# Kernel tuning notes

Hardware: AMD Instinct MI355X
Metric: run time of the kernel (lower is better)

The kernel has to match this reference:

```python
import jax, jax.numpy as jnp
import numpy as np

B, C = 65536, 1000
EPS = float(np.finfo(np.float32).eps)

def setup_inputs() -> dict:
    key = jax.random.key(0)
    k1, k2, k3 = jax.random.split(key, 3)
    return {
        "Simple_vector": jax.random.normal(k1, (B, C), dtype=jnp.float32),
        "label_list": jax.random.randint(k2, (B,), 0, C),
        "w_L": jax.random.normal(k3, (C,), dtype=jnp.float32),
        "w_H": jnp.ones((1,), dtype=jnp.float32),
        "b": jnp.ones((1,), dtype=jnp.float32),
    }

def reference(Simple_vector, label_list, w_L, w_H, b):
    C_ = Simple_vector.shape[1]
    # LTS: per-row dot with class-weight vector
    LTS = Simple_vector @ w_L  # (B,)
    # H_hat = sum_i p_i * log p_i  (negative entropy), single stable pass
    logp = jax.nn.log_softmax(Simple_vector, axis=1)
    H_hat = jnp.sum(jnp.exp(logp) * logp, axis=1)  # (B,)
    HTS = w_H[0] * (H_hat / jnp.log(jnp.float32(C_))) + b[0]
    a = LTS + HTS
    T = jnp.clip(jax.nn.softplus(a), EPS, None)  # (B,)
    scaled = Simple_vector / T[:, None]
    # mean cross-entropy
    ls = jax.nn.log_softmax(scaled, axis=1)
    nll = -jnp.take_along_axis(ls, label_list[:, None], axis=1)[:, 0]
    return jnp.mean(nll)
```

## Files before the change

kernel.cpp:

```cpp
#include <hip/hip_runtime.h>
#include <float.h>
#include <math.h>


static constexpr int   kC4    = 250;
static constexpr int   kBlock = 256;
static constexpr int   kGrid  = 2048;
static constexpr int   kWavesTotal = kGrid * (kBlock / 64);
static constexpr int   kRPW   = 8;
static constexpr float kEps   = 1.1920928955078125e-07f;
static constexpr float kLogC  = 6.907755279f;

__device__ __forceinline__ float wred_max(float v) {
#pragma unroll
  for (int off = 32; off > 0; off >>= 1) v = fmaxf(v, __shfl_xor(v, off, 64));
  return v;
}
__device__ __forceinline__ float wred_sum(float v) {
#pragma unroll
  for (int off = 32; off > 0; off >>= 1) v += __shfl_xor(v, off, 64);
  return v;
}

__device__ __forceinline__ void p1_dot_max(const float4 c, const float4 w,
                                           float& L, float& m) {
  L = fmaf(c.x, w.x, L); L = fmaf(c.y, w.y, L);
  L = fmaf(c.z, w.z, L); L = fmaf(c.w, w.w, L);
  m = fmaxf(m, fmaxf(fmaxf(c.x, c.y), fmaxf(c.z, c.w)));
}
__device__ __forceinline__ void p2_raw(const float4 c, float& S, float& W) {
  float e;
  e = __expf(c.x); S += e; W = fmaf(e, c.x, W);
  e = __expf(c.y); S += e; W = fmaf(e, c.y, W);
  e = __expf(c.z); S += e; W = fmaf(e, c.z, W);
  e = __expf(c.w); S += e; W = fmaf(e, c.w, W);
}
__device__ __forceinline__ void p3_sumexp2(const float4 c, const float rT,
                                           const float nmrT, float& S2) {
  S2 += __expf(fmaf(c.x, rT, nmrT)); S2 += __expf(fmaf(c.y, rT, nmrT));
  S2 += __expf(fmaf(c.z, rT, nmrT)); S2 += __expf(fmaf(c.w, rT, nmrT));
}
__device__ __forceinline__ float pick_lab(const float4 v, const int el) {
  return (el == 0) ? v.x : (el == 1) ? v.y : (el == 2) ? v.z : v.w;
}

#define SENT4 make_float4(-FLT_MAX, -FLT_MAX, -FLT_MAX, -FLT_MAX)

__global__ __launch_bounds__(kBlock, 4) void ats_row_kernel_ns(
    const float* __restrict__ X, const int* __restrict__ labels,
    const float* __restrict__ wL, const float* __restrict__ wH,
    const float* __restrict__ bb, double* __restrict__ partial) {
  const int lane   = threadIdx.x & 63;
  const int wib    = threadIdx.x >> 6;
  const int wid    = blockIdx.x * (kBlock / 64) + wib;
  const bool tailok = lane < (kC4 - 192);

  const float4* WLr = reinterpret_cast<const float4*>(wL);
  const float4 w0 = WLr[lane];
  const float4 w1 = WLr[64 + lane];
  const float4 w2 = WLr[128 + lane];
  const float4 w3 = tailok ? WLr[192 + lane] : make_float4(0.f, 0.f, 0.f, 0.f);
  const float wH0 = wH[0];
  const float b0  = bb[0];

  double acc = 0.0;
  const int base = wid * kRPW;

  float4 a0, a1, a2, a3, b0_, b1_, b2_, b3_;
  int labA, labB;
  {
    const float4* Xa = reinterpret_cast<const float4*>(X) + (size_t)base * kC4;
    a0 = Xa[lane]; a1 = Xa[64 + lane]; a2 = Xa[128 + lane];
    a3 = tailok ? Xa[192 + lane] : SENT4;
    labA = labels[base];
    const float4* Xb = Xa + kC4;
    b0_ = Xb[lane]; b1_ = Xb[64 + lane]; b2_ = Xb[128 + lane];
    b3_ = tailok ? Xb[192 + lane] : SENT4;
    labB = labels[base + 1];
  }

  float4 pa0, pa1, pa2, pa3;
  float prT = 0.f, pnmrT = 0.f, pxl = 0.f;

#pragma unroll
  for (int i = 0; i < kRPW; ++i) {
    float4 n0 = SENT4, n1 = SENT4, n2 = SENT4, n3 = SENT4;
    int labN = 0;
    if (i + 2 < kRPW) {
      const float4* Xn =
          reinterpret_cast<const float4*>(X) + (size_t)(base + i + 2) * kC4;
      n0 = Xn[lane]; n1 = Xn[64 + lane]; n2 = Xn[128 + lane];
      n3 = tailok ? Xn[192 + lane] : SENT4;
      labN = labels[base + i + 2];
    }

    float L = 0.f, m = -FLT_MAX;
    p1_dot_max(a0, w0, L, m); p1_dot_max(a1, w1, L, m);
    p1_dot_max(a2, w2, L, m); p1_dot_max(a3, w3, L, m);

    float S = 0.f, W = 0.f;
    p2_raw(a0, S, W); p2_raw(a1, S, W);
    p2_raw(a2, S, W); p2_raw(a3, S, W);

    float S2p = 0.f;
    if (i > 0) {
      p3_sumexp2(pa0, prT, pnmrT, S2p); p3_sumexp2(pa1, prT, pnmrT, S2p);
      p3_sumexp2(pa2, prT, pnmrT, S2p); p3_sumexp2(pa3, prT, pnmrT, S2p);
    }

    const int c4l = labA >> 2;
    const int sl  = c4l >> 6, ln = c4l & 63, el = labA & 3;
    float4 v = (sl == 0) ? a0 : (sl == 1) ? a1 : (sl == 2) ? a2 : a3;
    const float xl = __shfl(pick_lab(v, el), ln, 64);

#pragma unroll
    for (int off = 32; off > 0; off >>= 1) {
      const float mo  = __shfl_xor(m,   off, 64);
      const float So  = __shfl_xor(S,   off, 64);
      const float Wo  = __shfl_xor(W,   off, 64);
      const float Lo  = __shfl_xor(L,   off, 64);
      const float S2o = __shfl_xor(S2p, off, 64);
      m = fmaxf(m, mo);
      S += So; W += Wo; L += Lo; S2p += S2o;
    }

    if (i > 0) acc += (double)(__logf(S2p) - fmaf(pxl, prT, pnmrT));

    const float Hhat = W / S - __logf(S);
    const float aT   = L + wH0 * (Hhat / kLogC) + b0;
    const float sp   = (aT > 0.f) ? (aT + log1pf(__expf(-aT)))
                                  : log1pf(__expf(aT));
    const float T    = fmaxf(sp, kEps);
    const float rT   = 1.0f / T;

    prT = rT; pnmrT = -m * rT; pxl = xl;
    pa0 = a0; pa1 = a1; pa2 = a2; pa3 = a3;

    a0 = b0_; a1 = b1_; a2 = b2_; a3 = b3_; labA = labB;
    b0_ = n0; b1_ = n1; b2_ = n2; b3_ = n3; labB = labN;
  }

  {
    float S2p = 0.f;
    p3_sumexp2(pa0, prT, pnmrT, S2p); p3_sumexp2(pa1, prT, pnmrT, S2p);
    p3_sumexp2(pa2, prT, pnmrT, S2p); p3_sumexp2(pa3, prT, pnmrT, S2p);
    S2p = wred_sum(S2p);
    acc += (double)(__logf(S2p) - fmaf(pxl, prT, pnmrT));
  }

  __shared__ double sacc[kBlock / 64];
  if (lane == 0) sacc[wib] = acc;
  __syncthreads();
  if (threadIdx.x == 0)
    partial[blockIdx.x] = (sacc[0] + sacc[1]) + (sacc[2] + sacc[3]);
}

__device__ __forceinline__ void p2_sumexp(const float4 c, const float m,
                                          float& S, float& W) {
  float e;
  e = __expf(c.x - m); S += e; W = fmaf(e, c.x, W);
  e = __expf(c.y - m); S += e; W = fmaf(e, c.y, W);
  e = __expf(c.z - m); S += e; W = fmaf(e, c.z, W);
  e = __expf(c.w - m); S += e; W = fmaf(e, c.w, W);
}
__device__ __forceinline__ float row_nll(
    const float4 c0, const float4 c1, const float4 c2, const float4 c3,
    const float4 w0, const float4 w1, const float4 w2, const float4 w3,
    const int labc, const float wH0, const float b0) {
  float L = 0.f, m = -FLT_MAX;
  p1_dot_max(c0, w0, L, m); p1_dot_max(c1, w1, L, m);
  p1_dot_max(c2, w2, L, m); p1_dot_max(c3, w3, L, m);
  m = wred_max(m);
  float S = 0.f, W = 0.f;
  p2_sumexp(c0, m, S, W); p2_sumexp(c1, m, S, W);
  p2_sumexp(c2, m, S, W); p2_sumexp(c3, m, S, W);
  S = wred_sum(S); W = wred_sum(W); L = wred_sum(L);
  const int c4l = labc >> 2;
  const int sl = c4l >> 6, ln = c4l & 63, el = labc & 3;
  float4 v = (sl == 0) ? c0 : (sl == 1) ? c1 : (sl == 2) ? c2 : c3;
  const float xl = __shfl(pick_lab(v, el), ln, 64);
  const float Hhat = W / S - m - __logf(S);
  const float a = L + wH0 * (Hhat / kLogC) + b0;
  const float sp = (a > 0.f) ? (a + log1pf(__expf(-a))) : log1pf(__expf(a));
  const float T = fmaxf(sp, kEps);
  const float rT = 1.0f / T, nmrT = -m * rT;
  float S2 = 0.f;
  p3_sumexp2(c0, rT, nmrT, S2); p3_sumexp2(c1, rT, nmrT, S2);
  p3_sumexp2(c2, rT, nmrT, S2); p3_sumexp2(c3, rT, nmrT, S2);
  S2 = wred_sum(S2);
  return __logf(S2) - fmaf(xl, rT, nmrT);
}

__global__ __launch_bounds__(kBlock) void ats_row_kernel_gen(
    const float* __restrict__ X, const int* __restrict__ labels,
    const float* __restrict__ wL, const float* __restrict__ wH,
    const float* __restrict__ bb, double* __restrict__ partial, int B) {
  const int lane   = threadIdx.x & 63;
  const int wib    = threadIdx.x >> 6;
  const int wid    = blockIdx.x * (kBlock / 64) + wib;
  const bool tailok = lane < (kC4 - 192);

  const float4* WLr = reinterpret_cast<const float4*>(wL);
  const float4 w0 = WLr[lane];
  const float4 w1 = WLr[64 + lane];
  const float4 w2 = WLr[128 + lane];
  const float4 w3 = tailok ? WLr[192 + lane] : make_float4(0.f, 0.f, 0.f, 0.f);
  const float wH0 = wH[0];
  const float b0  = bb[0];

  double acc = 0.0;
  int row = wid;
  float4 c0, c1, c2, c3;
  int labc = 0;
  if (row < B) {
    const float4* Xr = reinterpret_cast<const float4*>(X) + (size_t)row * kC4;
    c0 = Xr[lane]; c1 = Xr[64 + lane]; c2 = Xr[128 + lane];
    c3 = tailok ? Xr[192 + lane] : SENT4;
    labc = labels[row];
  }
  for (; row < B; row += kWavesTotal) {
    const int nrow = row + kWavesTotal;
    float4 n0 = SENT4, n1 = SENT4, n2 = SENT4, n3 = SENT4;
    int labn = 0;
    if (nrow < B) {
      const float4* Xn = reinterpret_cast<const float4*>(X) + (size_t)nrow * kC4;
      n0 = Xn[lane]; n1 = Xn[64 + lane]; n2 = Xn[128 + lane];
      n3 = tailok ? Xn[192 + lane] : SENT4;
      labn = labels[nrow];
    }
    acc += (double)row_nll(c0, c1, c2, c3, w0, w1, w2, w3, labc, wH0, b0);
    c0 = n0; c1 = n1; c2 = n2; c3 = n3; labc = labn;
  }
  __shared__ double sacc[kBlock / 64];
  if (lane == 0) sacc[wib] = acc;
  __syncthreads();
  if (threadIdx.x == 0)
    partial[blockIdx.x] = (sacc[0] + sacc[1]) + (sacc[2] + sacc[3]);
}

__global__ __launch_bounds__(256) void ats_final_kernel(
    const double* __restrict__ partial, float* __restrict__ out, int n, int B) {
  __shared__ double sdata[256];
  double a = 0.0;
  for (int i = threadIdx.x; i < n; i += 256) a += partial[i];
  sdata[threadIdx.x] = a;
  __syncthreads();
#pragma unroll
  for (int s = 128; s > 0; s >>= 1) {
    if ((int)threadIdx.x < s) sdata[threadIdx.x] += sdata[threadIdx.x + s];
    __syncthreads();
  }
  if (threadIdx.x == 0) out[0] = (float)(sdata[0] / (double)B);
}

extern "C" void kernel_launch(void* const* d_in, const int* in_sizes, int n_in,
                              void* d_out, int out_size, void* d_ws, size_t ws_size,
                              hipStream_t stream) {
  (void)n_in; (void)out_size; (void)ws_size;
  const float* X   = (const float*)d_in[0];
  const int*   lab = (const int*)d_in[1];
  const float* wL  = (const float*)d_in[2];
  const float* wH  = (const float*)d_in[3];
  const float* bb  = (const float*)d_in[4];
  const int B = in_sizes[1];
  double* partial = (double*)d_ws;
  float* out = (float*)d_out;

  if (B == kWavesTotal * kRPW) {
    ats_row_kernel_ns<<<kGrid, kBlock, 0, stream>>>(X, lab, wL, wH, bb, partial);
  } else {
    ats_row_kernel_gen<<<kGrid, kBlock, 0, stream>>>(X, lab, wL, wH, bb,
                                                     partial, B);
  }
  ats_final_kernel<<<1, 256, 0, stream>>>(partial, out, kGrid, B);
}
```

Baseline: 61.32 us.

## Cut register pressure: stage w_L in LDS, shallower prefetch, occupancy 5

Moves the class-weight vector from per-lane registers into shared memory and reloads it each row. The row prefetch depth drops from two rows ahead to one, and launch bounds are raised from 4 to 5 blocks per CU. Together these free registers so more waves can be resident to hide memory latency. The cost is extra LDS reads per row, a block-wide barrier at start, and less prefetch lookahead within each wave.

```diff
diff --git a/kernel.cpp b/kernel.cpp
--- a/kernel.cpp
+++ b/kernel.cpp
@@ -46,7 +46,7 @@
 
 #define SENT4 make_float4(-FLT_MAX, -FLT_MAX, -FLT_MAX, -FLT_MAX)
 
-__global__ __launch_bounds__(kBlock, 4) void ats_row_kernel_ns(
+__global__ __launch_bounds__(kBlock, 5) void ats_row_kernel_o5(
     const float* __restrict__ X, const int* __restrict__ labels,
     const float* __restrict__ wL, const float* __restrict__ wH,
     const float* __restrict__ bb, double* __restrict__ partial) {
@@ -55,28 +55,28 @@
   const int wid    = blockIdx.x * (kBlock / 64) + wib;
   const bool tailok = lane < (kC4 - 192);
 
-  const float4* WLr = reinterpret_cast<const float4*>(wL);
-  const float4 w0 = WLr[lane];
-  const float4 w1 = WLr[64 + lane];
-  const float4 w2 = WLr[128 + lane];
-  const float4 w3 = tailok ? WLr[192 + lane] : make_float4(0.f, 0.f, 0.f, 0.f);
+  __shared__ float4 sWL[256];
+  {
+    const float4* WLr = reinterpret_cast<const float4*>(wL);
+    if ((int)threadIdx.x < kC4) sWL[threadIdx.x] = WLr[threadIdx.x];
+    if (threadIdx.x >= kC4 && threadIdx.x < 256)
+      sWL[threadIdx.x] = make_float4(0.f, 0.f, 0.f, 0.f);
+  }
+  __syncthreads();
+
   const float wH0 = wH[0];
   const float b0  = bb[0];
 
   double acc = 0.0;
   const int base = wid * kRPW;
 
-  float4 a0, a1, a2, a3, b0_, b1_, b2_, b3_;
-  int labA, labB;
+  float4 a0, a1, a2, a3;
+  int labA;
   {
     const float4* Xa = reinterpret_cast<const float4*>(X) + (size_t)base * kC4;
     a0 = Xa[lane]; a1 = Xa[64 + lane]; a2 = Xa[128 + lane];
     a3 = tailok ? Xa[192 + lane] : SENT4;
     labA = labels[base];
-    const float4* Xb = Xa + kC4;
-    b0_ = Xb[lane]; b1_ = Xb[64 + lane]; b2_ = Xb[128 + lane];
-    b3_ = tailok ? Xb[192 + lane] : SENT4;
-    labB = labels[base + 1];
   }
 
   float4 pa0, pa1, pa2, pa3;
@@ -86,13 +86,18 @@
   for (int i = 0; i < kRPW; ++i) {
     float4 n0 = SENT4, n1 = SENT4, n2 = SENT4, n3 = SENT4;
     int labN = 0;
-    if (i + 2 < kRPW) {
+    if (i + 1 < kRPW) {
       const float4* Xn =
-          reinterpret_cast<const float4*>(X) + (size_t)(base + i + 2) * kC4;
+          reinterpret_cast<const float4*>(X) + (size_t)(base + i + 1) * kC4;
       n0 = Xn[lane]; n1 = Xn[64 + lane]; n2 = Xn[128 + lane];
       n3 = tailok ? Xn[192 + lane] : SENT4;
-      labN = labels[base + i + 2];
-    }
+      labN = labels[base + i + 1];
+    }
+
+    const float4 w0 = sWL[lane];
+    const float4 w1 = sWL[64 + lane];
+    const float4 w2 = sWL[128 + lane];
+    const float4 w3 = sWL[192 + lane];
 
     float L = 0.f, m = -FLT_MAX;
     p1_dot_max(a0, w0, L, m); p1_dot_max(a1, w1, L, m);
@@ -136,8 +141,7 @@
     prT = rT; pnmrT = -m * rT; pxl = xl;
     pa0 = a0; pa1 = a1; pa2 = a2; pa3 = a3;
 
-    a0 = b0_; a1 = b1_; a2 = b2_; a3 = b3_; labA = labB;
-    b0_ = n0; b1_ = n1; b2_ = n2; b3_ = n3; labB = labN;
+    a0 = n0; a1 = n1; a2 = n2; a3 = n3; labA = labN;
   }
 
   {
@@ -267,7 +271,7 @@
   float* out = (float*)d_out;
 
   if (B == kWavesTotal * kRPW) {
-    ats_row_kernel_ns<<<kGrid, kBlock, 0, stream>>>(X, lab, wL, wH, bb, partial);
+    ats_row_kernel_o5<<<kGrid, kBlock, 0, stream>>>(X, lab, wL, wH, bb, partial);
   } else {
     ats_row_kernel_gen<<<kGrid, kBlock, 0, stream>>>(X, lab, wL, wH, bb,
                                                      partial, B);
```

After: 66.30 us. 8.1% more time.
